# Performance work log

Hardware: AMD Instinct MI355X
Metric: run time of the kernel (lower is better)

## Reference

```python
import jax, jax.numpy as jnp
import numpy as np

EPS = 1e-6
MOMENTUM = 0.9


def _normalize(x, eps=EPS):
    # Matches torch F.normalize: x / clamp_min(||x||, eps)
    n = jnp.linalg.norm(x, axis=-1, keepdims=True)
    return x / jnp.maximum(n, eps)


def setup_inputs() -> dict:
    key = jax.random.key(0)
    k1, k2 = jax.random.split(key)
    embeddings = jax.random.normal(k1, (131072, 512), dtype=jnp.float32)
    prototypes = jax.random.normal(k2, (1024, 512), dtype=jnp.float32)
    return {"embeddings": embeddings, "prototypes": prototypes}


def reference(embeddings, prototypes):
    # Steady-state update path of PrototypeBank.update (filled == bank_size).
    K = prototypes.shape[0]
    e = _normalize(embeddings)                      # [N, D]
    active = _normalize(prototypes)                 # [K, D]
    sims = jnp.einsum('nd,kd->nk', e, active)       # [N, K]
    assign = jnp.argmax(sims, axis=1)               # [N] int
    # per-prototype masked mean via segment reduction
    sums = jax.ops.segment_sum(e, assign, num_segments=K)          # [K, D]
    counts = jax.ops.segment_sum(jnp.ones((e.shape[0],), e.dtype), assign,
                                 num_segments=K)                    # [K]
    has = counts > 0
    cluster_mean = sums / jnp.maximum(counts, 1.0)[:, None]
    # EMA uses the RAW stored prototype (not the normalized copy), then renormalizes
    updated = MOMENTUM * prototypes + (1.0 - MOMENTUM) * cluster_mean
    updated = _normalize(updated)
    new_prototypes = jnp.where(has[:, None], updated, prototypes)
    return new_prototypes
```

## Files before the change

### kernel.cpp

```cpp
#include <hip/hip_runtime.h>


#define D 512
#define NPROTO 1024
#define ROWS 64

typedef __attribute__((ext_vector_type(8)))  unsigned short ushort8;
typedef __attribute__((ext_vector_type(8)))  __bf16 bfrag8;
typedef __attribute__((ext_vector_type(16))) float f32x16;

static __device__ inline unsigned short f2bf(float f) {
    unsigned int u = __float_as_uint(f);
    u = u + 0x7FFFu + ((u >> 16) & 1u);
    return (unsigned short)(u >> 16);
}

__global__ __launch_bounds__(256) void norm_protos_kernel(
    const float* __restrict__ protos, unsigned short* __restrict__ pbf,
    int* __restrict__ counts, float* __restrict__ psum)
{
    const int wave = threadIdx.x >> 6, lane = threadIdx.x & 63;
    const int row = blockIdx.x * 4 + wave;
    const float* src = protos + (size_t)row * D + lane * 8;
    float4 v0 = *(const float4*)src;
    float4 v1 = *(const float4*)(src + 4);
    float ss = v0.x*v0.x + v0.y*v0.y + v0.z*v0.z + v0.w*v0.w
             + v1.x*v1.x + v1.y*v1.y + v1.z*v1.z + v1.w*v1.w;
    #pragma unroll
    for (int off = 32; off > 0; off >>= 1) ss += __shfl_xor(ss, off, 64);
    const float inv = 1.0f / fmaxf(sqrtf(ss), 1e-6f);
    ushort8 w;
    w[0] = f2bf(v0.x*inv); w[1] = f2bf(v0.y*inv); w[2] = f2bf(v0.z*inv); w[3] = f2bf(v0.w*inv);
    w[4] = f2bf(v1.x*inv); w[5] = f2bf(v1.y*inv); w[6] = f2bf(v1.z*inv); w[7] = f2bf(v1.w*inv);
    const size_t dst = (size_t)(row >> 5) * 16384 + (lane >> 1) * 512
                     + (lane & 1) * 256 + (row & 31) * 8;
    *(ushort8*)(pbf + dst) = w;
    const int gid = blockIdx.x * 256 + threadIdx.x;
    const float4 z = make_float4(0.f, 0.f, 0.f, 0.f);
    ((float4*)psum)[gid * 2]     = z;
    ((float4*)psum)[gid * 2 + 1] = z;
    if (blockIdx.x == 0) ((int4*)counts)[threadIdx.x] = (int4){0, 0, 0, 0};
}

__global__ __launch_bounds__(512, 4) void assign_kernel(
    const float* __restrict__ emb, const unsigned short* __restrict__ pbf,
    int* __restrict__ assign, float* __restrict__ invnorm, int* __restrict__ counts)
{
    __shared__ __align__(16) unsigned short eT[ROWS * D];
    __shared__ float swmax[8][64];
    __shared__ int   swidx[8][64];
    const int tid = threadIdx.x;
    const int wave = tid >> 6, lane = tid & 63;
    const int rowbase = blockIdx.x * ROWS;
    const int c32 = lane & 31, h = lane >> 5;

    for (int rr = 0; rr < 8; ++rr) {
        const int rloc = wave * 8 + rr;
        const float* src = emb + (size_t)(rowbase + rloc) * D + lane * 8;
        float4 v0 = *(const float4*)src;
        float4 v1 = *(const float4*)(src + 4);
        float ss = v0.x*v0.x + v0.y*v0.y + v0.z*v0.z + v0.w*v0.w
                 + v1.x*v1.x + v1.y*v1.y + v1.z*v1.z + v1.w*v1.w;
        #pragma unroll
        for (int off = 32; off > 0; off >>= 1) ss += __shfl_xor(ss, off, 64);
        if (lane == 0) invnorm[rowbase + rloc] = 1.0f / fmaxf(sqrtf(ss), 1e-6f);
        ushort8 w;
        w[0] = f2bf(v0.x); w[1] = f2bf(v0.y); w[2] = f2bf(v0.z); w[3] = f2bf(v0.w);
        w[4] = f2bf(v1.x); w[5] = f2bf(v1.y); w[6] = f2bf(v1.z); w[7] = f2bf(v1.w);
        const int slot = lane ^ (rloc & 7);
        *(ushort8*)(&eT[rloc * D + slot * 8]) = w;
    }
    __syncthreads();

    float rv0 = -3.4e38f, rv1 = -3.4e38f;
    int   ri0 = 0,        ri1 = 0;

    const int bbase0 = c32 * D;
    const int bbase1 = (32 + c32) * D;
    const int rxor = c32 & 7;

    for (int ng = 0; ng < 2; ++ng) {
        const int pbase = ng * 512 + wave * 64;
        const unsigned short* pa0 = pbf + (size_t)(pbase >> 5) * 16384 + lane * 8;
        const unsigned short* pa1 = pa0 + 16384;

        f32x16 acc00 = (f32x16)(0.f), acc01 = (f32x16)(0.f);
        f32x16 acc10 = (f32x16)(0.f), acc11 = (f32x16)(0.f);

        #pragma unroll 8
        for (int ks = 0; ks < 32; ++ks) {
            const bfrag8 a0 = *(const bfrag8*)(pa0 + ks * 512);
            const bfrag8 a1 = *(const bfrag8*)(pa1 + ks * 512);
            const int slot = ((ks * 2 + h) ^ rxor) * 8;
            const bfrag8 b0 = *(const bfrag8*)(&eT[bbase0 + slot]);
            const bfrag8 b1 = *(const bfrag8*)(&eT[bbase1 + slot]);
            acc00 = __builtin_amdgcn_mfma_f32_32x32x16_bf16(a0, b0, acc00, 0, 0, 0);
            acc01 = __builtin_amdgcn_mfma_f32_32x32x16_bf16(a0, b1, acc01, 0, 0, 0);
            acc10 = __builtin_amdgcn_mfma_f32_32x32x16_bf16(a1, b0, acc10, 0, 0, 0);
            acc11 = __builtin_amdgcn_mfma_f32_32x32x16_bf16(a1, b1, acc11, 0, 0, 0);
        }

        float bv0 = -3.4e38f, bv1 = -3.4e38f;
        int   bi0 = 0,        bi1 = 0;
        #pragma unroll
        for (int j = 0; j < 16; ++j) {
            const int row = (j & 3) + 8 * (j >> 2) + 4 * h;
            const float v0 = acc00[j], v1 = acc01[j];
            if (v0 > bv0) { bv0 = v0; bi0 = pbase + row; }
            if (v1 > bv1) { bv1 = v1; bi1 = pbase + row; }
        }
        #pragma unroll
        for (int j = 0; j < 16; ++j) {
            const int row = 32 + (j & 3) + 8 * (j >> 2) + 4 * h;
            const float v0 = acc10[j], v1 = acc11[j];
            if (v0 > bv0) { bv0 = v0; bi0 = pbase + row; }
            if (v1 > bv1) { bv1 = v1; bi1 = pbase + row; }
        }
        {
            const float ov = __shfl_xor(bv0, 32, 64);
            const int   oi = __shfl_xor(bi0, 32, 64);
            if (ov > bv0 || (ov == bv0 && oi < bi0)) { bv0 = ov; bi0 = oi; }
        }
        {
            const float ov = __shfl_xor(bv1, 32, 64);
            const int   oi = __shfl_xor(bi1, 32, 64);
            if (ov > bv1 || (ov == bv1 && oi < bi1)) { bv1 = ov; bi1 = oi; }
        }
        if (bv0 > rv0) { rv0 = bv0; ri0 = bi0; }
        if (bv1 > rv1) { rv1 = bv1; ri1 = bi1; }
    }

    if (h == 0) {
        swmax[wave][c32]      = rv0;  swidx[wave][c32]      = ri0;
        swmax[wave][32 + c32] = rv1;  swidx[wave][32 + c32] = ri1;
    }
    __syncthreads();

    if (tid < 64) {
        float v = swmax[0][tid]; int idx = swidx[0][tid];
        #pragma unroll
        for (int w = 1; w < 8; ++w) {
            const float ov = swmax[w][tid];
            const int   oi = swidx[w][tid];
            if (ov > v || (ov == v && oi < idx)) { v = ov; idx = oi; }
        }
        assign[rowbase + tid] = idx;
        atomicAdd(&counts[idx], 1);
    }
}

__global__ __launch_bounds__(1024) void prefix_kernel(
    const int* __restrict__ counts, int* __restrict__ offsets,
    int* __restrict__ cursor, int* __restrict__ items, int* __restrict__ nitems)
{
    __shared__ unsigned wtot[16];
    const int t = threadIdx.x;
    const int lane = t & 63, wv = t >> 6;
    const int c = counts[t];
    const int nseg = (c + 255) >> 8;
    unsigned v = (unsigned)c | ((unsigned)nseg << 20);
    #pragma unroll
    for (int off = 1; off < 64; off <<= 1) {
        const unsigned n = __shfl_up(v, off, 64);
        if (lane >= off) v += n;
    }
    if (lane == 63) wtot[wv] = v;
    __syncthreads();
    if (t < 16) {
        unsigned x = wtot[t];
        #pragma unroll
        for (int off = 1; off < 16; off <<= 1) {
            const unsigned n = __shfl_up(x, off, 16);
            if (t >= off) x += n;
        }
        wtot[t] = x;
    }
    __syncthreads();
    if (wv > 0) v += wtot[wv - 1];
    const int incl_c = (int)(v & 0xFFFFFu);
    const int incl_s = (int)(v >> 20);
    const int excl = incl_c - c;
    offsets[t] = excl;
    cursor[t]  = excl;
    const int segexcl = incl_s - nseg;
    for (int s = 0; s < nseg; ++s) items[segexcl + s] = (t << 12) | s;
    if (t == NPROTO - 1) *nitems = incl_s;
}

__global__ __launch_bounds__(256) void scatter_kernel(
    const int* __restrict__ assign, int* __restrict__ cursor, int* __restrict__ bin)
{
    const int i = blockIdx.x * 256 + threadIdx.x;
    const int k = assign[i];
    const int pos = atomicAdd(&cursor[k], 1);
    bin[pos] = i;
}

__global__ __launch_bounds__(256) void psum_kernel(
    const float* __restrict__ emb, const int* __restrict__ bin,
    const int* __restrict__ counts, const int* __restrict__ offsets,
    const float* __restrict__ invnorm, const int* __restrict__ items,
    const int* __restrict__ nitems, float* __restrict__ psum)
{
    if ((int)blockIdx.x >= *nitems) return;
    __shared__ float4 part[128];
    __shared__ int   sidx[256];
    __shared__ float sinv[256];
    const int item = items[blockIdx.x];
    const int k = item >> 12, seg = item & 4095;
    const int off = offsets[k], cnt = counts[k];
    const int s0 = seg * 256;
    const int n = min(256, cnt - s0);
    const int t = threadIdx.x;

    if (t < n) {
        const int r = bin[off + s0 + t];
        sidx[t] = r;
        sinv[t] = invnorm[r];
    }
    __syncthreads();

    const int par = t >> 7, colg = (t & 127) * 4;
    float4 acc = make_float4(0.f, 0.f, 0.f, 0.f);
    #pragma unroll 4
    for (int j = par; j < n; j += 2) {
        const int r = sidx[j];
        const float sc = sinv[j];
        const float4 v = *(const float4*)(emb + (size_t)r * D + colg);
        acc.x += v.x * sc; acc.y += v.y * sc; acc.z += v.z * sc; acc.w += v.w * sc;
    }

    if (par == 1) part[t & 127] = acc;
    __syncthreads();
    if (par == 0) {
        const float4 o = part[t];
        float* dst = psum + (size_t)k * D + colg;
        atomicAdd(dst + 0, acc.x + o.x);
        atomicAdd(dst + 1, acc.y + o.y);
        atomicAdd(dst + 2, acc.z + o.z);
        atomicAdd(dst + 3, acc.w + o.w);
    }
}

__global__ __launch_bounds__(128) void final_kernel(
    const float* __restrict__ protos, const float* __restrict__ psum,
    const int* __restrict__ counts, float* __restrict__ out)
{
    __shared__ float red[2];
    const int k = blockIdx.x, t = threadIdx.x;
    const int colg = t * 4;
    const int cnt = counts[k];
    const float denom = fmaxf((float)cnt, 1.0f);
    const float4 s  = *(const float4*)(psum + (size_t)k * D + colg);
    const float4 p4 = *(const float4*)(protos + (size_t)k * D + colg);
    float4 u;
    u.x = 0.9f * p4.x + 0.1f * s.x / denom;
    u.y = 0.9f * p4.y + 0.1f * s.y / denom;
    u.z = 0.9f * p4.z + 0.1f * s.z / denom;
    u.w = 0.9f * p4.w + 0.1f * s.w / denom;
    float ss = u.x*u.x + u.y*u.y + u.z*u.z + u.w*u.w;
    #pragma unroll
    for (int off = 32; off > 0; off >>= 1) ss += __shfl_xor(ss, off, 64);
    if ((t & 63) == 0) red[t >> 6] = ss;
    __syncthreads();
    const float tot = red[0] + red[1];
    const float inv = 1.0f / fmaxf(sqrtf(tot), 1e-6f);
    float4 o;
    o.x = (cnt > 0) ? u.x * inv : p4.x;
    o.y = (cnt > 0) ? u.y * inv : p4.y;
    o.z = (cnt > 0) ? u.z * inv : p4.z;
    o.w = (cnt > 0) ? u.w * inv : p4.w;
    *(float4*)(out + (size_t)k * D + colg) = o;
}

extern "C" void kernel_launch(void* const* d_in, const int* in_sizes, int n_in,
                              void* d_out, int out_size, void* d_ws, size_t ws_size,
                              hipStream_t stream)
{
    const float* emb    = (const float*)d_in[0];
    const float* protos = (const float*)d_in[1];
    float* out = (float*)d_out;
    const int n_emb = in_sizes[0] / D;

    char* ws = (char*)d_ws;
    unsigned short* pbf = (unsigned short*)ws;
    int*   assign  = (int*)  (ws + (1 << 20));
    float* invnorm = (float*)(ws + (1 << 20) + (512 << 10));
    int*   counts  = (int*)  (ws + (2 << 20));
    int*   offsets = (int*)  (ws + (2 << 20) + (4 << 10));
    int*   cursor  = (int*)  (ws + (2 << 20) + (8 << 10));
    int*   nitems  = (int*)  (ws + (2 << 20) + (12 << 10));
    int*   items   = (int*)  (ws + (2 << 20) + (16 << 10));
    int*   bin     = (int*)  (ws + (2 << 20) + (24 << 10));
    float* psum    = (float*)(ws + (2 << 20) + (24 << 10) + (512 << 10));

    norm_protos_kernel<<<NPROTO / 4, 256, 0, stream>>>(protos, pbf, counts, psum);
    assign_kernel<<<n_emb / ROWS, 512, 0, stream>>>(emb, pbf, assign, invnorm, counts);
    prefix_kernel<<<1, 1024, 0, stream>>>(counts, offsets, cursor, items, nitems);
    scatter_kernel<<<n_emb / 256, 256, 0, stream>>>(assign, cursor, bin);
    psum_kernel<<<1536, 256, 0, stream>>>(emb, bin, counts, offsets, invnorm,
                                          items, nitems, psum);
    final_kernel<<<NPROTO, 128, 0, stream>>>(protos, psum, counts, out);
}
```

Measured before the change: 529.5 us.

## Stream prototype fragments into per-wave LDS ring via async global_load_lds

The assign kernel now prefetches the bf16 prototype fragments into a per-wave 5-deep LDS ring buffer using global_load_lds, issuing loads 4 k-steps ahead and waiting with explicit vmcnt counts before each MFMA step. The first fragments are issued before the embedding staging so their latency overlaps the normalization phase. The goal is to hide the global-memory latency of the A operand, which was previously loaded straight into registers inside the MFMA loop. In exchange, LDS use per block rises by about 80KB and the occupancy hint in launch_bounds is dropped, so fewer blocks may fit per CU. The k loops are also fully unrolled.

Result: slower. 574.6 us (+8.5%).

```diff
diff --git a/kernel.cpp b/kernel.cpp
--- a/kernel.cpp
+++ b/kernel.cpp
@@ -4,6 +4,7 @@
 #define D 512
 #define NPROTO 1024
 #define ROWS 64
+#define DEPTH 5
 
 typedef __attribute__((ext_vector_type(8)))  unsigned short ushort8;
 typedef __attribute__((ext_vector_type(8)))  __bf16 bfrag8;
@@ -13,6 +14,13 @@
     unsigned int u = __float_as_uint(f);
     u = u + 0x7FFFu + ((u >> 16) & 1u);
     return (unsigned short)(u >> 16);
+}
+
+static __device__ __forceinline__ void gload16(const unsigned short* g,
+                                               unsigned short* l) {
+    __builtin_amdgcn_global_load_lds(
+        (const __attribute__((address_space(1))) unsigned int*)g,
+        (__attribute__((address_space(3))) unsigned int*)l, 16, 0, 0);
 }
 
 __global__ __launch_bounds__(256) void norm_protos_kernel(
@@ -42,17 +50,28 @@
     if (blockIdx.x == 0) ((int4*)counts)[threadIdx.x] = (int4){0, 0, 0, 0};
 }
 
-__global__ __launch_bounds__(512, 4) void assign_kernel(
+__global__ __launch_bounds__(512) void assign_kernel(
     const float* __restrict__ emb, const unsigned short* __restrict__ pbf,
     int* __restrict__ assign, float* __restrict__ invnorm, int* __restrict__ counts)
 {
     __shared__ __align__(16) unsigned short eT[ROWS * D];
+    __shared__ __align__(16) unsigned short aring[8 * DEPTH * 1024];
     __shared__ float swmax[8][64];
     __shared__ int   swidx[8][64];
     const int tid = threadIdx.x;
     const int wave = tid >> 6, lane = tid & 63;
     const int rowbase = blockIdx.x * ROWS;
     const int c32 = lane & 31, h = lane >> 5;
+
+    const unsigned short* gA = pbf + (size_t)wave * 32768 + lane * 8;
+    unsigned short* awu = aring + wave * (DEPTH * 1024);
+
+    #pragma unroll
+    for (int kk = 0; kk < 4; ++kk) {
+        const unsigned short* g0 = gA + kk * 512;
+        gload16(g0,         awu + kk * 1024);
+        gload16(g0 + 16384, awu + kk * 1024 + 512);
+    }
 
     for (int rr = 0; rr < 8; ++rr) {
         const int rloc = wave * 8 + rr;
@@ -79,18 +98,28 @@
     const int bbase1 = (32 + c32) * D;
     const int rxor = c32 & 7;
 
+    #pragma unroll
     for (int ng = 0; ng < 2; ++ng) {
         const int pbase = ng * 512 + wave * 64;
-        const unsigned short* pa0 = pbf + (size_t)(pbase >> 5) * 16384 + lane * 8;
-        const unsigned short* pa1 = pa0 + 16384;
 
         f32x16 acc00 = (f32x16)(0.f), acc01 = (f32x16)(0.f);
         f32x16 acc10 = (f32x16)(0.f), acc11 = (f32x16)(0.f);
 
-        #pragma unroll 8
+        #pragma unroll
         for (int ks = 0; ks < 32; ++ks) {
-            const bfrag8 a0 = *(const bfrag8*)(pa0 + ks * 512);
-            const bfrag8 a1 = *(const bfrag8*)(pa1 + ks * 512);
+            const int kk = ng * 32 + ks;
+            {
+                const int kkn = kk + 4;
+                const int kkc = kkn > 63 ? 63 : kkn;
+                const unsigned short* g0 = gA + (kkc >> 5) * 262144 + (kkc & 31) * 512;
+                unsigned short* ld = awu + (kkn % DEPTH) * 1024;
+                gload16(g0,         ld);
+                gload16(g0 + 16384, ld + 512);
+            }
+            asm volatile("s_waitcnt vmcnt(8)" ::: "memory");
+            const unsigned short* ar = awu + (kk % DEPTH) * 1024;
+            const bfrag8 a0 = *(const bfrag8*)(ar + lane * 8);
+            const bfrag8 a1 = *(const bfrag8*)(ar + 512 + lane * 8);
             const int slot = ((ks * 2 + h) ^ rxor) * 8;
             const bfrag8 b0 = *(const bfrag8*)(&eT[bbase0 + slot]);
             const bfrag8 b1 = *(const bfrag8*)(&eT[bbase1 + slot]);
@@ -129,6 +158,8 @@
         if (bv0 > rv0) { rv0 = bv0; ri0 = bi0; }
         if (bv1 > rv1) { rv1 = bv1; ri1 = bi1; }
     }
+
+    asm volatile("s_waitcnt vmcnt(0)" ::: "memory");
 
     if (h == 0) {
         swmax[wave][c32]      = rv0;  swidx[wave][c32]      = ri0;
```
